# Performance work log

Hardware: AMD Instinct MI355X
Metric: run time of the kernel (lower is better)

The kernel has to match this reference:

```python
import jax, jax.numpy as jnp
import numpy as np


def setup_inputs() -> dict:
    key = jax.random.key(0)
    k1, k2 = jax.random.split(key)
    latent = jax.random.normal(k1, (131072, 128), dtype=jnp.float32)
    coords = jax.random.normal(k2, (2048, 128), dtype=jnp.float32)
    return {"latent": latent, "coords": coords}


def reference(latent, coords):
    # torch.cdist(latent, coords).min(1)[1]
    # argmin over euclidean distance == argmin over squared distance,
    # so we skip the sqrt (same result, cheaper and numerically safer).
    x2 = jnp.sum(latent * latent, axis=1, keepdims=True)          # [N, 1]
    c2 = jnp.sum(coords * coords, axis=1)                          # [C]
    cross = latent @ coords.T                                      # [N, C]
    d2 = x2 + c2[None, :] - 2.0 * cross                            # [N, C] squared dists
    return jnp.argmin(d2, axis=1)                                  # [N] int indices
```

## Files before the change

### kernel.cpp

```cpp
#include <hip/hip_runtime.h>


constexpr int D = 128;
constexpr int C = 2048;
constexpr int NCH = 64;
constexpr int NCHUNKS = C / NCH;
constexpr float MARGIN_H = 0.01f;
constexpr int WL_CAP = 32768;

constexpr size_t WS_CNT = 8192;
constexpr size_t WS_WL  = 16384;
constexpr size_t WS_BH  = 262144;
constexpr size_t WS_BL  = 786432;

typedef __attribute__((ext_vector_type(8))) short short8;
typedef __attribute__((ext_vector_type(4))) float f32x4;
typedef unsigned int u32;

__device__ inline unsigned short bf16_rne(float x) {
    unsigned u = __float_as_uint(x);
    u += 0x7FFFu + ((u >> 16) & 1u);
    return (unsigned short)(u >> 16);
}
__device__ inline float bf16_to_f(unsigned short h) {
    return __uint_as_float(((unsigned)h) << 16);
}
__device__ inline void split8(const float* v, short8* hi, short8* lo) {
#pragma unroll
    for (int j = 0; j < 8; ++j) {
        unsigned short h = bf16_rne(v[j]);
        (*hi)[j] = (short)h;
        (*lo)[j] = (short)bf16_rne(v[j] - bf16_to_f(h));
    }
}

__device__ __forceinline__ void gl_lds16(const void* g, void* l) {
    __builtin_amdgcn_global_load_lds(
        (const __attribute__((address_space(1))) u32*)g,
        (__attribute__((address_space(3))) u32*)l, 16, 0, 0);
}

__global__ void prep_coords(const float* __restrict__ coords,
                            unsigned short* __restrict__ Bh,
                            unsigned short* __restrict__ Bl,
                            float* __restrict__ c2, int* __restrict__ counter) {
    int t = blockIdx.x * blockDim.x + threadIdx.x;
    if (t == 0) *counter = 0;
    if (t >= C * 16) return;
    int c  = t >> 4;
    int k8 = t & 15;
    float v[8];
    *(float4*)(v)     = *(const float4*)(coords + (size_t)c * D + k8 * 8);
    *(float4*)(v + 4) = *(const float4*)(coords + (size_t)c * D + k8 * 8 + 4);
    short8 hi, lo;
    split8(v, &hi, &lo);
    int ch = c >> 6, nl = c & 63;
    size_t off = (size_t)ch * (NCH * 128) + ((size_t)nl * 16 + (k8 ^ (nl & 15))) * 8;
    *(short8*)(Bh + off) = hi;
    *(short8*)(Bl + off) = lo;
    float p = 0.f;
#pragma unroll
    for (int j = 0; j < 8; ++j) p = fmaf(v[j], v[j], p);
#pragma unroll
    for (int m = 1; m <= 8; m <<= 1) p += __shfl_xor(p, m, 64);
    if (k8 == 0) c2[c] = p;
}


__global__ __launch_bounds__(256, 2) void centroid_fast(
        const float* __restrict__ latent,
        const unsigned short* __restrict__ Bh_img,
        const unsigned short* __restrict__ Bl_img,
        const float* __restrict__ c2g,
        int* __restrict__ out,
        int* __restrict__ counter,
        int* __restrict__ worklist) {
    __shared__ __align__(16) unsigned short Bh[2][NCH * 128], Bl[2][NCH * 128];
    __shared__ __align__(16) float sc2[C];

    const int tid  = threadIdx.x;
    const int wid  = tid >> 6;
    const int lane = tid & 63;
    const int q    = lane >> 4, lr = lane & 15;
    const int row_block = blockIdx.x * 256;

    if ((blockIdx.x ^ (blockIdx.x >> 8)) & 1) {
#pragma unroll
        for (int i = 0; i < 14; ++i) __builtin_amdgcn_s_sleep(8);
    }

    {
        const unsigned short* sh = Bh_img;
        const unsigned short* sl = Bl_img;
#pragma unroll
        for (int i = 0; i < 4; ++i) {
            int e = (i * 256 + tid) * 8;
            gl_lds16(sh + e, &Bh[0][e]);
            gl_lds16(sl + e, &Bl[0][e]);
        }
    }
#pragma unroll
    for (int i = 0; i < 2; ++i) {
        int e = (i * 256 + tid) * 4;
        *(float4*)(sc2 + e) = *(const float4*)(c2g + e);
    }

    short8 Ah[4][4], Al[4][4];
#pragma unroll
    for (int mt = 0; mt < 4; ++mt) {
        const float* rp = latent + (size_t)(row_block + wid * 64 + mt * 16 + lr) * D;
#pragma unroll
        for (int ks = 0; ks < 4; ++ks) {
            float v[8];
            *(float4*)(v)     = *(const float4*)(rp + ks * 32 + q * 8);
            *(float4*)(v + 4) = *(const float4*)(rp + ks * 32 + q * 8 + 4);
            split8(v, &Ah[mt][ks], &Al[mt][ks]);
        }
    }

    float b1[16], b2[16];
    int   bidx[16];
#pragma unroll
    for (int s = 0; s < 16; ++s) { b1[s] = -3.4e38f; b2[s] = -3.4e38f; bidx[s] = 0; }

    __syncthreads();

    for (int ch = 0; ch < NCHUNKS; ++ch) {
        const int buf = ch & 1;
        if (ch + 1 < NCHUNKS) {
            const unsigned short* sh = Bh_img + (size_t)(ch + 1) * (NCH * 128);
            const unsigned short* sl = Bl_img + (size_t)(ch + 1) * (NCH * 128);
#pragma unroll
            for (int i = 0; i < 4; ++i) {
                int e = (i * 256 + tid) * 8;
                gl_lds16(sh + e, &Bh[buf ^ 1][e]);
                gl_lds16(sl + e, &Bl[buf ^ 1][e]);
            }
            asm volatile("s_waitcnt vmcnt(8)" ::: "memory");
        } else {
            asm volatile("s_waitcnt vmcnt(0)" ::: "memory");
        }
        __builtin_amdgcn_s_barrier();

#pragma unroll
        for (int nt = 0; nt < 4; ++nt) {
            const int nl = nt * 16 + lr;
            const float mh = -0.5f * sc2[ch * NCH + nl];
            f32x4 acc[4];
#pragma unroll
            for (int mt = 0; mt < 4; ++mt) acc[mt] = (f32x4){mh, mh, mh, mh};
            __builtin_amdgcn_s_setprio(1);
#pragma unroll
            for (int ks = 0; ks < 4; ++ks) {
                const int xv = ((ks * 4) | q) ^ lr;
                const int e  = nl * 128 + xv * 8;
                short8 bh = *(const short8*)(&Bh[buf][e]);
                short8 bl = *(const short8*)(&Bl[buf][e]);
#pragma unroll
                for (int mt = 0; mt < 4; ++mt)
                    acc[mt] = __builtin_amdgcn_mfma_f32_16x16x32_bf16(Ah[mt][ks], bh, acc[mt], 0, 0, 0);
#pragma unroll
                for (int mt = 0; mt < 4; ++mt)
                    acc[mt] = __builtin_amdgcn_mfma_f32_16x16x32_bf16(Ah[mt][ks], bl, acc[mt], 0, 0, 0);
#pragma unroll
                for (int mt = 0; mt < 4; ++mt)
                    acc[mt] = __builtin_amdgcn_mfma_f32_16x16x32_bf16(Al[mt][ks], bh, acc[mt], 0, 0, 0);
            }
            __builtin_amdgcn_s_setprio(0);
            const int n_global = ch * NCH + nl;
#pragma unroll
            for (int mt = 0; mt < 4; ++mt)
#pragma unroll
                for (int r = 0; r < 4; ++r) {
                    int slot = mt * 4 + r;
                    float a = acc[mt][r];
                    b2[slot]   = __builtin_amdgcn_fmed3f(a, b1[slot], b2[slot]);
                    bool gt    = a > b1[slot];
                    b1[slot]   = fmaxf(a, b1[slot]);
                    bidx[slot] = gt ? n_global : bidx[slot];
                }
        }
        __builtin_amdgcn_s_barrier();
    }

#pragma unroll
    for (int m = 1; m <= 8; m <<= 1) {
#pragma unroll
        for (int s = 0; s < 16; ++s) {
            float oa = __shfl_xor(b1[s], m, 64);
            float ob = __shfl_xor(b2[s], m, 64);
            int   oi = __shfl_xor(bidx[s], m, 64);
            float mn = fminf(b1[s], oa);
            b2[s] = fmaxf(fmaxf(b2[s], ob), mn);
            bool take = oa > b1[s];
            b1[s]   = take ? oa : b1[s];
            bidx[s] = take ? oi : bidx[s];
        }
    }
#pragma unroll
    for (int s = 0; s < 16; ++s) {
        if (lr == s) {
            int row = row_block + wid * 64 + (s >> 2) * 16 + q * 4 + (s & 3);
            out[row] = bidx[s];
            if (b1[s] - b2[s] < MARGIN_H) {
                int w = atomicAdd(counter, 1);
                if (w < WL_CAP) worklist[w] = row;
            }
        }
    }
}


__global__ __launch_bounds__(256) void refine_fp64(
        const float* __restrict__ latent, const float* __restrict__ coords,
        const int* __restrict__ worklist, const int* __restrict__ counter,
        int wl_cap, int* __restrict__ out) {
    __shared__ float  xs[D];
    __shared__ double rv[256];
    __shared__ int    ri[256];

    int n = *counter;
    if (n > wl_cap) n = wl_cap;

    for (int wi = blockIdx.x; wi < n; wi += gridDim.x) {
        int row = worklist[wi];
        if (threadIdx.x < D)
            xs[threadIdx.x] = latent[(size_t)row * D + threadIdx.x];
        __syncthreads();

        double best = 1.0e300;
        int    bix  = 0;
        for (int c = threadIdx.x; c < C; c += 256) {
            const float4* cp = (const float4*)(coords + (size_t)c * D);
            double s0 = 0.0, s1 = 0.0, s2 = 0.0, s3 = 0.0;
#pragma unroll 8
            for (int k4 = 0; k4 < 32; ++k4) {
                float4 v = cp[k4];
                double d0 = (double)xs[k4 * 4 + 0] - (double)v.x;
                double d1 = (double)xs[k4 * 4 + 1] - (double)v.y;
                double d2 = (double)xs[k4 * 4 + 2] - (double)v.z;
                double d3 = (double)xs[k4 * 4 + 3] - (double)v.w;
                s0 = fma(d0, d0, s0); s1 = fma(d1, d1, s1);
                s2 = fma(d2, d2, s2); s3 = fma(d3, d3, s3);
            }
            double s = (s0 + s1) + (s2 + s3);
            if (s < best) { best = s; bix = c; }
        }
        rv[threadIdx.x] = best;
        ri[threadIdx.x] = bix;
        __syncthreads();
        for (int off = 128; off > 0; off >>= 1) {
            if (threadIdx.x < off) {
                double ov = rv[threadIdx.x + off];
                int    oi = ri[threadIdx.x + off];
                if (ov < rv[threadIdx.x] ||
                    (ov == rv[threadIdx.x] && oi < ri[threadIdx.x])) {
                    rv[threadIdx.x] = ov;
                    ri[threadIdx.x] = oi;
                }
            }
            __syncthreads();
        }
        if (threadIdx.x == 0) out[row] = ri[0];
        __syncthreads();
    }
}

extern "C" void kernel_launch(void* const* d_in, const int* in_sizes, int n_in,
                              void* d_out, int out_size, void* d_ws, size_t ws_size,
                              hipStream_t stream) {
    const float* latent = (const float*)d_in[0];
    const float* coords = (const float*)d_in[1];
    int*         out    = (int*)d_out;

    char* ws = (char*)d_ws;
    float* c2      = (float*)ws;
    int*   counter = (int*)(ws + WS_CNT);
    int*   wl      = (int*)(ws + WS_WL);
    unsigned short* Bh = (unsigned short*)(ws + WS_BH);
    unsigned short* Bl = (unsigned short*)(ws + WS_BL);
    const int n_rows = in_sizes[0] / D;

    prep_coords<<<(C * 16) / 256, 256, 0, stream>>>(coords, Bh, Bl, c2, counter);
    centroid_fast<<<n_rows / 256, 256, 0, stream>>>(latent, Bh, Bl, c2, out,
                                                    counter, wl);
    refine_fp64<<<608, 256, 0, stream>>>(latent, coords, wl, counter, WL_CAP, out);
}
```

Measured before the change: 292.7 us.

## Replace split-bf16 MFMA distance GEMM with two-level int8 quantized MFMA

Switches the screening GEMM from a three-product bf16 hi/lo split to a per-row scaled int8 hi/lo decomposition using i32 16x16x64 int8 MFMAs, with the scales and -0.5*c2 packed into a float2 per centroid. This halves LDS and global traffic for the centroid tiles, halves the K-steps per tile, and uses the higher int8 MFMA throughput. In exchange it adds a dequantize FMA per accumulator element and changes the error profile. The existing margin-based fp64 refine pass must still catch near-ties, so the refine worklist may grow.

```diff
diff --git a/kernel.cpp b/kernel.cpp
--- a/kernel.cpp
+++ b/kernel.cpp
@@ -8,30 +8,25 @@
 constexpr float MARGIN_H = 0.01f;
 constexpr int WL_CAP = 32768;
 
-constexpr size_t WS_CNT = 8192;
-constexpr size_t WS_WL  = 16384;
+constexpr size_t WS_CNT = 16384;
+constexpr size_t WS_WL  = 32768;
 constexpr size_t WS_BH  = 262144;
-constexpr size_t WS_BL  = 786432;
-
-typedef __attribute__((ext_vector_type(8))) short short8;
-typedef __attribute__((ext_vector_type(4))) float f32x4;
+constexpr size_t WS_BL  = 524288;
+
+typedef __attribute__((ext_vector_type(4))) int   i32x4;
 typedef unsigned int u32;
 
-__device__ inline unsigned short bf16_rne(float x) {
-    unsigned u = __float_as_uint(x);
-    u += 0x7FFFu + ((u >> 16) & 1u);
-    return (unsigned short)(u >> 16);
-}
-__device__ inline float bf16_to_f(unsigned short h) {
-    return __uint_as_float(((unsigned)h) << 16);
-}
-__device__ inline void split8(const float* v, short8* hi, short8* lo) {
-#pragma unroll
-    for (int j = 0; j < 8; ++j) {
-        unsigned short h = bf16_rne(v[j]);
-        (*hi)[j] = (short)h;
-        (*lo)[j] = (short)bf16_rne(v[j] - bf16_to_f(h));
-    }
+__device__ __forceinline__ int pack4(int a0, int a1, int a2, int a3) {
+    return (int)(((u32)a0 & 255u) | (((u32)a1 & 255u) << 8) |
+                 (((u32)a2 & 255u) << 16) | (((u32)a3 & 255u) << 24));
+}
+
+__device__ __forceinline__ void q2(float v, float qa, float inv, float inv128,
+                                   int* h, int* l) {
+    float hf = __builtin_rintf(v * inv);
+    *h = (int)hf;
+    float r = fmaf(-hf, qa, v);
+    *l = (int)__builtin_rintf(r * inv128);
 }
 
 __device__ __forceinline__ void gl_lds16(const void* g, void* l) {
@@ -41,42 +36,66 @@
 }
 
 __global__ void prep_coords(const float* __restrict__ coords,
-                            unsigned short* __restrict__ Bh,
-                            unsigned short* __restrict__ Bl,
-                            float* __restrict__ c2, int* __restrict__ counter) {
+                            signed char* __restrict__ Bh,
+                            signed char* __restrict__ Bl,
+                            float2* __restrict__ qc2, int* __restrict__ counter) {
     int t = blockIdx.x * blockDim.x + threadIdx.x;
     if (t == 0) *counter = 0;
-    if (t >= C * 16) return;
-    int c  = t >> 4;
-    int k8 = t & 15;
-    float v[8];
-    *(float4*)(v)     = *(const float4*)(coords + (size_t)c * D + k8 * 8);
-    *(float4*)(v + 4) = *(const float4*)(coords + (size_t)c * D + k8 * 8 + 4);
-    short8 hi, lo;
-    split8(v, &hi, &lo);
+    if (t >= C * 4) return;
+    int c = t >> 2, p = t & 3;
+    float v[32];
+#pragma unroll
+    for (int i = 0; i < 8; ++i)
+        *(float4*)(v + i * 4) = *(const float4*)(coords + (size_t)c * D + p * 32 + i * 4);
+    float amax = 0.f, ss = 0.f;
+#pragma unroll
+    for (int j = 0; j < 32; ++j) {
+        amax = fmaxf(amax, fabsf(v[j]));
+        ss = fmaf(v[j], v[j], ss);
+    }
+#pragma unroll
+    for (int m = 1; m <= 2; m <<= 1) {
+        amax = fmaxf(amax, __shfl_xor(amax, m, 64));
+        ss += __shfl_xor(ss, m, 64);
+    }
+    float qb = fmaxf(amax, 1e-30f) * (1.f / 127.f);
+    float inv = 127.f / fmaxf(amax, 1e-30f);
+    float inv128 = inv * 128.f;
+
     int ch = c >> 6, nl = c & 63;
-    size_t off = (size_t)ch * (NCH * 128) + ((size_t)nl * 16 + (k8 ^ (nl & 15))) * 8;
-    *(short8*)(Bh + off) = hi;
-    *(short8*)(Bl + off) = lo;
-    float p = 0.f;
-#pragma unroll
-    for (int j = 0; j < 8; ++j) p = fmaf(v[j], v[j], p);
-#pragma unroll
-    for (int m = 1; m <= 8; m <<= 1) p += __shfl_xor(p, m, 64);
-    if (k8 == 0) c2[c] = p;
+    size_t cbase = (size_t)ch * (NCH * 128) + (size_t)nl * 128;
+#pragma unroll
+    for (int g = 0; g < 2; ++g) {
+        int g8 = p * 2 + g;
+        int hw[4], lw[4];
+#pragma unroll
+        for (int w = 0; w < 4; ++w) {
+            int h0, l0, h1, l1, h2, l2, h3, l3;
+            q2(v[g * 16 + w * 4 + 0], qb, inv, inv128, &h0, &l0);
+            q2(v[g * 16 + w * 4 + 1], qb, inv, inv128, &h1, &l1);
+            q2(v[g * 16 + w * 4 + 2], qb, inv, inv128, &h2, &l2);
+            q2(v[g * 16 + w * 4 + 3], qb, inv, inv128, &h3, &l3);
+            hw[w] = pack4(h0, h1, h2, h3);
+            lw[w] = pack4(l0, l1, l2, l3);
+        }
+        size_t off = cbase + (size_t)(g8 ^ (nl & 7)) * 16;
+        *(i32x4*)(Bh + off) = (i32x4){hw[0], hw[1], hw[2], hw[3]};
+        *(i32x4*)(Bl + off) = (i32x4){lw[0], lw[1], lw[2], lw[3]};
+    }
+    if (p == 0) qc2[c] = make_float2(qb, -0.5f * ss);
 }
 
 
 __global__ __launch_bounds__(256, 2) void centroid_fast(
         const float* __restrict__ latent,
-        const unsigned short* __restrict__ Bh_img,
-        const unsigned short* __restrict__ Bl_img,
-        const float* __restrict__ c2g,
+        const signed char* __restrict__ Bh_img,
+        const signed char* __restrict__ Bl_img,
+        const float2* __restrict__ qc2g,
         int* __restrict__ out,
         int* __restrict__ counter,
         int* __restrict__ worklist) {
-    __shared__ __align__(16) unsigned short Bh[2][NCH * 128], Bl[2][NCH * 128];
-    __shared__ __align__(16) float sc2[C];
+    __shared__ __align__(16) signed char Bh[2][NCH * 128], Bl[2][NCH * 128];
+    __shared__ __align__(16) float2 sqc[C];
 
     const int tid  = threadIdx.x;
     const int wid  = tid >> 6;
@@ -89,33 +108,57 @@
         for (int i = 0; i < 14; ++i) __builtin_amdgcn_s_sleep(8);
     }
 
-    {
-        const unsigned short* sh = Bh_img;
-        const unsigned short* sl = Bl_img;
-#pragma unroll
-        for (int i = 0; i < 4; ++i) {
-            int e = (i * 256 + tid) * 8;
-            gl_lds16(sh + e, &Bh[0][e]);
-            gl_lds16(sl + e, &Bl[0][e]);
-        }
-    }
 #pragma unroll
     for (int i = 0; i < 2; ++i) {
-        int e = (i * 256 + tid) * 4;
-        *(float4*)(sc2 + e) = *(const float4*)(c2g + e);
-    }
-
-    short8 Ah[4][4], Al[4][4];
+        int e = (i * 256 + tid) * 16;
+        gl_lds16(Bh_img + e, &Bh[0][e]);
+        gl_lds16(Bl_img + e, &Bl[0][e]);
+    }
+#pragma unroll
+    for (int i = 0; i < 4; ++i) {
+        int e = (i * 256 + tid) * 2;
+        *(float4*)(&sqc[e]) = *(const float4*)(&qc2g[e]);
+    }
+
+    i32x4 Ah[4][2], Al[4][2];
+    float qAr[4][4];
 #pragma unroll
     for (int mt = 0; mt < 4; ++mt) {
         const float* rp = latent + (size_t)(row_block + wid * 64 + mt * 16 + lr) * D;
-#pragma unroll
-        for (int ks = 0; ks < 4; ++ks) {
-            float v[8];
-            *(float4*)(v)     = *(const float4*)(rp + ks * 32 + q * 8);
-            *(float4*)(v + 4) = *(const float4*)(rp + ks * 32 + q * 8 + 4);
-            split8(v, &Ah[mt][ks], &Al[mt][ks]);
-        }
+        float v[32];
+#pragma unroll
+        for (int ks = 0; ks < 2; ++ks)
+#pragma unroll
+            for (int i = 0; i < 4; ++i)
+                *(float4*)(v + ks * 16 + i * 4) =
+                    *(const float4*)(rp + ks * 64 + q * 16 + i * 4);
+        float amax = 0.f;
+#pragma unroll
+        for (int j = 0; j < 32; ++j) amax = fmaxf(amax, fabsf(v[j]));
+        amax = fmaxf(amax, __shfl_xor(amax, 16, 64));
+        amax = fmaxf(amax, __shfl_xor(amax, 32, 64));
+        float qa = fmaxf(amax, 1e-30f) * (1.f / 127.f);
+        float inv = 127.f / fmaxf(amax, 1e-30f);
+        float inv128 = inv * 128.f;
+#pragma unroll
+        for (int ks = 0; ks < 2; ++ks) {
+            int hw[4], lw[4];
+#pragma unroll
+            for (int w = 0; w < 4; ++w) {
+                int h0, l0, h1, l1, h2, l2, h3, l3;
+                q2(v[ks * 16 + w * 4 + 0], qa, inv, inv128, &h0, &l0);
+                q2(v[ks * 16 + w * 4 + 1], qa, inv, inv128, &h1, &l1);
+                q2(v[ks * 16 + w * 4 + 2], qa, inv, inv128, &h2, &l2);
+                q2(v[ks * 16 + w * 4 + 3], qa, inv, inv128, &h3, &l3);
+                hw[w] = pack4(h0, h1, h2, h3);
+                lw[w] = pack4(l0, l1, l2, l3);
+            }
+            Ah[mt][ks] = (i32x4){hw[0], hw[1], hw[2], hw[3]};
+            Al[mt][ks] = (i32x4){lw[0], lw[1], lw[2], lw[3]};
+        }
+#pragma unroll
+        for (int r = 0; r < 4; ++r)
+            qAr[mt][r] = __shfl(qa, (lane & 48) | (q * 4 + r), 64);
     }
 
     float b1[16], b2[16];
@@ -127,16 +170,17 @@
 
     for (int ch = 0; ch < NCHUNKS; ++ch) {
         const int buf = ch & 1;
+        const int chbase = ch * NCH;
         if (ch + 1 < NCHUNKS) {
-            const unsigned short* sh = Bh_img + (size_t)(ch + 1) * (NCH * 128);
-            const unsigned short* sl = Bl_img + (size_t)(ch + 1) * (NCH * 128);
-#pragma unroll
-            for (int i = 0; i < 4; ++i) {
-                int e = (i * 256 + tid) * 8;
+            const signed char* sh = Bh_img + (size_t)(ch + 1) * (NCH * 128);
+            const signed char* sl = Bl_img + (size_t)(ch + 1) * (NCH * 128);
+#pragma unroll
+            for (int i = 0; i < 2; ++i) {
+                int e = (i * 256 + tid) * 16;
                 gl_lds16(sh + e, &Bh[buf ^ 1][e]);
                 gl_lds16(sl + e, &Bl[buf ^ 1][e]);
             }
-            asm volatile("s_waitcnt vmcnt(8)" ::: "memory");
+            asm volatile("s_waitcnt vmcnt(4)" ::: "memory");
         } else {
             asm volatile("s_waitcnt vmcnt(0)" ::: "memory");
         }
@@ -145,35 +189,38 @@
 #pragma unroll
         for (int nt = 0; nt < 4; ++nt) {
             const int nl = nt * 16 + lr;
-            const float mh = -0.5f * sc2[ch * NCH + nl];
-            f32x4 acc[4];
-#pragma unroll
-            for (int mt = 0; mt < 4; ++mt) acc[mt] = (f32x4){mh, mh, mh, mh};
+            const float2 qc = sqc[chbase + nl];
+            i32x4 I1[4], I2[4];
+#pragma unroll
+            for (int mt = 0; mt < 4; ++mt) {
+                I1[mt] = (i32x4){0, 0, 0, 0};
+                I2[mt] = (i32x4){0, 0, 0, 0};
+            }
             __builtin_amdgcn_s_setprio(1);
 #pragma unroll
-            for (int ks = 0; ks < 4; ++ks) {
-                const int xv = ((ks * 4) | q) ^ lr;
-                const int e  = nl * 128 + xv * 8;
-                short8 bh = *(const short8*)(&Bh[buf][e]);
-                short8 bl = *(const short8*)(&Bl[buf][e]);
+            for (int ks = 0; ks < 2; ++ks) {
+                const int e = nl * 128 + (((ks << 2) | q) ^ (lr & 7)) * 16;
+                i32x4 bh = *(const i32x4*)(&Bh[buf][e]);
+                i32x4 bl = *(const i32x4*)(&Bl[buf][e]);
 #pragma unroll
                 for (int mt = 0; mt < 4; ++mt)
-                    acc[mt] = __builtin_amdgcn_mfma_f32_16x16x32_bf16(Ah[mt][ks], bh, acc[mt], 0, 0, 0);
+                    I1[mt] = __builtin_amdgcn_mfma_i32_16x16x64_i8(Ah[mt][ks], bh, I1[mt], 0, 0, 0);
 #pragma unroll
                 for (int mt = 0; mt < 4; ++mt)
-                    acc[mt] = __builtin_amdgcn_mfma_f32_16x16x32_bf16(Ah[mt][ks], bl, acc[mt], 0, 0, 0);
+                    I2[mt] = __builtin_amdgcn_mfma_i32_16x16x64_i8(Ah[mt][ks], bl, I2[mt], 0, 0, 0);
 #pragma unroll
                 for (int mt = 0; mt < 4; ++mt)
-                    acc[mt] = __builtin_amdgcn_mfma_f32_16x16x32_bf16(Al[mt][ks], bh, acc[mt], 0, 0, 0);
+                    I2[mt] = __builtin_amdgcn_mfma_i32_16x16x64_i8(Al[mt][ks], bh, I2[mt], 0, 0, 0);
             }
             __builtin_amdgcn_s_setprio(0);
-            const int n_global = ch * NCH + nl;
+            const int n_global = chbase + nl;
 #pragma unroll
             for (int mt = 0; mt < 4; ++mt)
 #pragma unroll
                 for (int r = 0; r < 4; ++r) {
                     int slot = mt * 4 + r;
-                    float a = acc[mt][r];
+                    float x = fmaf((float)I2[mt][r], 0.0078125f, (float)I1[mt][r]);
+                    float a = fmaf(qAr[mt][r], x * qc.x, qc.y);
                     b2[slot]   = __builtin_amdgcn_fmed3f(a, b1[slot], b2[slot]);
                     bool gt    = a > b1[slot];
                     b1[slot]   = fmaxf(a, b1[slot]);
@@ -274,15 +321,15 @@
     int*         out    = (int*)d_out;
 
     char* ws = (char*)d_ws;
-    float* c2      = (float*)ws;
-    int*   counter = (int*)(ws + WS_CNT);
-    int*   wl      = (int*)(ws + WS_WL);
-    unsigned short* Bh = (unsigned short*)(ws + WS_BH);
-    unsigned short* Bl = (unsigned short*)(ws + WS_BL);
+    float2* qc2    = (float2*)ws;
+    int*    counter = (int*)(ws + WS_CNT);
+    int*    wl      = (int*)(ws + WS_WL);
+    signed char* Bh = (signed char*)(ws + WS_BH);
+    signed char* Bl = (signed char*)(ws + WS_BL);
     const int n_rows = in_sizes[0] / D;
 
-    prep_coords<<<(C * 16) / 256, 256, 0, stream>>>(coords, Bh, Bl, c2, counter);
-    centroid_fast<<<n_rows / 256, 256, 0, stream>>>(latent, Bh, Bl, c2, out,
+    prep_coords<<<(C * 4) / 256, 256, 0, stream>>>(coords, Bh, Bl, qc2, counter);
+    centroid_fast<<<n_rows / 256, 256, 0, stream>>>(latent, Bh, Bl, qc2, out,
                                                     counter, wl);
     refine_fp64<<<608, 256, 0, stream>>>(latent, coords, wl, counter, WL_CAP, out);
 }
```

Result: faster. 276.3 us (-5.6%).
